# Performance work log

Measured on AMD Instinct MI355X. Metric: run time of the kernel, lower is better.

Reference implementation:

```python
import jax, jax.numpy as jnp
import numpy as np

R, N, E = 6, 50000, 200000
D, H, C, O = 768, 4, 64, 64  # input_dim, heads, hidden_dim1, output_dim


def _gatv2(x, src, tgt, Wl_r, Wr_r, att_r, b_r):
    # PyG GATv2Conv (concat=True, add_self_loops=True, negative_slope=0.2)
    n = x.shape[0]
    xl = (x @ Wl_r).reshape(n, H, C)  # source transform (lin_l)
    xr = (x @ Wr_r).reshape(n, H, C)  # target transform (lin_r)
    loops = jnp.arange(n, dtype=src.dtype)
    s = jnp.concatenate([src, loops])
    t = jnp.concatenate([tgt, loops])
    e = jax.nn.leaky_relu(xl[s] + xr[t], 0.2)          # [E+N, H, C]
    logits = jnp.einsum('ehc,hc->eh', e, att_r)         # [E+N, H]
    m = jax.ops.segment_max(logits, t, num_segments=n)  # softmax over incoming edges
    a = jnp.exp(logits - m[t])
    denom = jax.ops.segment_sum(a, t, num_segments=n)
    alpha = a / (denom[t] + 1e-16)
    msg = xl[s] * alpha[:, :, None]                     # [E+N, H, C]
    out = jax.ops.segment_sum(msg, t, num_segments=n)
    return out.reshape(n, H * C) + b_r


def _graphconv(x, src, tgt, W_rel, W_root, b):
    # PyG GraphConv (aggr='add'): lin_rel(sum_j x_j) + lin_root(x)
    agg = jax.ops.segment_sum(x[src], tgt, num_segments=x.shape[0])
    return agg @ W_rel + b + x @ W_root


def setup_inputs() -> dict:
    key = jax.random.key(0)
    ks = jax.random.split(key, 12)
    s = 0.05
    return {
        'x': jax.random.normal(ks[0], (N, D), jnp.float32),
        'edge_index': jax.random.randint(ks[1], (R, 2, E), 0, N, jnp.int32),
        'Wl': jax.random.normal(ks[2], (R, D, H * C), jnp.float32) * s,
        'Wr': jax.random.normal(ks[3], (R, D, H * C), jnp.float32) * s,
        'att': jax.random.normal(ks[4], (R, H, C), jnp.float32) * s,
        'b_gat': jax.random.normal(ks[5], (R, H * C), jnp.float32) * s,
        'W_rel1': jax.random.normal(ks[6], (R, H * C, C), jnp.float32) * s,
        'W_root1': jax.random.normal(ks[7], (R, H * C, C), jnp.float32) * s,
        'b1': jax.random.normal(ks[8], (R, C), jnp.float32) * s,
        'W_rel2': jax.random.normal(ks[9], (R, C, O), jnp.float32) * s,
        'W_root2': jax.random.normal(ks[10], (R, C, O), jnp.float32) * s,
        'b2': jax.random.normal(ks[11], (R, O), jnp.float32) * s,
    }


def reference(x, edge_index, Wl, Wr, att, b_gat, W_rel1, W_root1, b1, W_rel2, W_root2, b2):
    outs = []
    for r in range(R):  # fixed small set of structurally distinct relation towers
        src, tgt = edge_index[r, 0], edge_index[r, 1]
        h = _gatv2(x, src, tgt, Wl[r], Wr[r], att[r], b_gat[r])
        h = jax.nn.relu(h)
        h = jax.nn.relu(_graphconv(h, src, tgt, W_rel1[r], W_root1[r], b1[r]))
        h = _graphconv(h, src, tgt, W_rel2[r], W_root2[r], b2[r])
        outs.append(h)
    return jnp.stack(outs, axis=1)  # [N, R, O]
```

## Files before the change

kernel.cpp:

```cpp
#include <hip/hip_runtime.h>
#include <hip/hip_bf16.h>
#include <math.h>

#define RREL 6
#define NN   50000
#define EE   200000
#define DD   768
#define HH   4
#define CC   64
#define HC   256
#define OO   64
#define MPAD 50176
#define SCAN_B 49
#define NT   12

typedef __attribute__((ext_vector_type(8))) short short8;
typedef __attribute__((ext_vector_type(4))) float f32x4;
typedef __attribute__((ext_vector_type(8))) unsigned short ushort8v;
typedef __attribute__((ext_vector_type(4))) unsigned short ushort4v;

__device__ __forceinline__ float b2f(unsigned short u) {
  return __uint_as_float(((unsigned)u) << 16);
}
__device__ __forceinline__ unsigned short f2b(float f) {
  __hip_bfloat16 h = __float2bfloat16(f);
  unsigned short u;
  __builtin_memcpy(&u, &h, 2);
  return u;
}

__device__ __forceinline__ void gload16(const void* g, void* s) {
  typedef __attribute__((address_space(1))) void gvoid;
  typedef __attribute__((address_space(3))) void svoid;
  __builtin_amdgcn_global_load_lds((gvoid*)(unsigned long long)g,
                                   (svoid*)(unsigned long long)s, 16, 0, 0);
}

__global__ __launch_bounds__(256) void k_cvt_x(const float* __restrict__ x,
                                               unsigned short* __restrict__ xb) {
  long t = (long)blockIdx.x * 256 + threadIdx.x;
  long base = t * 8;
  int row = (int)(base / DD);
  ushort8v o;
  if (row < NN) {
    float4 a = *(const float4*)(x + base);
    float4 b = *(const float4*)(x + base + 4);
    o[0] = f2b(a.x); o[1] = f2b(a.y); o[2] = f2b(a.z); o[3] = f2b(a.w);
    o[4] = f2b(b.x); o[5] = f2b(b.y); o[6] = f2b(b.z); o[7] = f2b(b.w);
  } else {
    o = (ushort8v)0;
  }
  *(ushort8v*)(xb + base) = o;
}

__global__ __launch_bounds__(256) void k_repack_w(const float* __restrict__ Wl,
                                                  const float* __restrict__ Wr,
                                                  unsigned short* __restrict__ Wt) {
  __shared__ float t[32][33];
  int k0 = blockIdx.x * 32, j0 = blockIdx.y * 32, r = blockIdx.z;
  int tx = threadIdx.x & 31, ty = threadIdx.x >> 5;
#pragma unroll
  for (int s = 0; s < 4; s++) {
    int k = k0 + ty + 8 * s, j = j0 + tx;
    float v = (j < HC) ? Wl[((long)r * DD + k) * HC + j]
                       : Wr[((long)r * DD + k) * HC + (j - HC)];
    t[ty + 8 * s][tx] = v;
  }
  __syncthreads();
#pragma unroll
  for (int s = 0; s < 4; s++) {
    int j = j0 + ty + 8 * s, k = k0 + tx;
    Wt[((long)r * 512 + j) * DD + k] = f2b(t[tx][ty + 8 * s]);
  }
}

__global__ void k_repack_gc(const float* __restrict__ Wrel, const float* __restrict__ Wroot,
                            unsigned short* __restrict__ Bt, int K) {
  int idx = blockIdx.x * blockDim.x + threadIdx.x;
  if (idx >= RREL * 64 * K) return;
  int k = idx % K;
  int o = (idx / K) % 64;
  int r = idx / (64 * K);
  int h = K >> 1;
  float v = (k < h) ? Wrel[((long)r * h + k) * 64 + o]
                    : Wroot[((long)r * h + (k - h)) * 64 + o];
  Bt[idx] = f2b(v);
}

#define STAGE_A(HALF, TT)                                                              \
  if ((TT) < NT) {                                                                     \
    long ko = (long)(TT) * 128;                                                        \
    char* db = ldsA + (((TT) & 1) << 15);                                              \
    gload16(AgB + (long)((HALF) * 64 + rA) * 1536 + ko + xcol,                         \
            db + ((HALF) * 64) * 128 + wave * 1024);                                   \
    gload16(AgB + (long)((HALF) * 64 + 128 + rA) * 1536 + ko + xcol,                   \
            db + ((HALF) * 64 + 128) * 128 + wave * 1024);                             \
  }

#define STAGE_B(HALF, TT)                                                              \
  if ((TT) < NT) {                                                                     \
    long ko = (long)(TT) * 128;                                                        \
    char* db = ldsB + (((TT) & 1) << 15);                                              \
    gload16(BgB + (long)(rb0 + (HALF) * 32 + lane8) * 1536 + ko + xcol,                \
            db + (rb0 + (HALF) * 32) * 128);                                           \
    gload16(BgB + (long)(rb1 + (HALF) * 32 + lane8) * 1536 + ko + xcol,                \
            db + (rb1 + (HALF) * 32) * 128);                                           \
  }

#define RD_PA(MH)                                                                      \
  do {                                                                                 \
    _Pragma("unroll") for (int fi = 0; fi < 4; ++fi) {                                 \
      pa[fi][0] = *(const short8*)(Ard + ((MH) * 64 + fi * 16) * 128 + s0);            \
      pa[fi][1] = *(const short8*)(Ard + ((MH) * 64 + fi * 16) * 128 + s1);            \
    }                                                                                  \
  } while (0)

#define RD_PB(NH)                                                                      \
  do {                                                                                 \
    _Pragma("unroll") for (int fj = 0; fj < 2; ++fj) {                                 \
      pb[fj][0] = *(const short8*)(Brd + ((NH) * 32 + fj * 16) * 128 + s0);            \
      pb[fj][1] = *(const short8*)(Brd + ((NH) * 32 + fj * 16) * 128 + s1);            \
    }                                                                                  \
  } while (0)

#define MM8(MH, NH)                                                                    \
  do {                                                                                 \
    _Pragma("unroll") for (int fi = 0; fi < 4; ++fi)                                   \
    _Pragma("unroll") for (int fj = 0; fj < 2; ++fj) {                                 \
      f32x4 c = acc[(MH) * 4 + fi][(NH) * 2 + fj];                                     \
      c = __builtin_amdgcn_mfma_f32_16x16x32_bf16(pa[fi][0], pb[fj][0], c, 0, 0, 0);   \
      c = __builtin_amdgcn_mfma_f32_16x16x32_bf16(pa[fi][1], pb[fj][1], c, 0, 0, 0);   \
      acc[(MH) * 4 + fi][(NH) * 2 + fj] = c;                                           \
    }                                                                                  \
  } while (0)

__global__ __launch_bounds__(512, 2) void k_gemm(const short* __restrict__ A,
                                                 const short* __restrict__ Bt,
                                                 unsigned short* __restrict__ Yall) {
  __shared__ __align__(16) char ldsA[65536];
  __shared__ __align__(16) char ldsB[65536];
  int tid = threadIdx.x;
  int wgid = blockIdx.x;
  int swz = (wgid & 7) * 294 + (wgid >> 3);
  int bm = swz / 12, bn = swz % 12;
  int lane = tid & 63, wave = tid >> 6;
  int warp_m = wave >> 2, warp_n = wave & 3;
  int wm = warp_m * 128, wn = warp_n * 64;
  int l16 = lane & 15, quad = lane >> 4;
  int gm0 = bm * 256;
  const char* AgB = (const char*)A + (long)gm0 * 1536;
  const char* BgB = (const char*)Bt + (long)bn * 256 * 1536;
  int rA = tid >> 3;
  int lane8 = lane >> 3;
  long xcol = (long)(((tid & 7) ^ (rA & 7)) * 16);
  int rb0 = (wave >> 2) * 64 + (wave & 3) * 8;
  int rb1 = rb0 + 128;
  int s0 = (quad ^ (l16 & 7)) * 16, s1 = s0 ^ 64;
  f32x4 acc[8][4] = {};

  STAGE_A(0, 0); STAGE_B(0, 0); STAGE_A(1, 0); STAGE_B(1, 0);
  STAGE_A(0, 1); STAGE_B(0, 1);
  asm volatile("s_waitcnt vmcnt(4)" ::: "memory");
  __builtin_amdgcn_s_barrier();

  for (int t = 0; t < NT; ++t) {
    int bo = (t & 1) << 15;
    const char* Ard = ldsA + bo + (wm + l16) * 128;
    const char* Brd = ldsB + bo + (wn + l16) * 128;
    short8 pa[4][2], pb[2][2];
    STAGE_A(1, t + 1);
    RD_PA(0); RD_PB(0);
    __builtin_amdgcn_s_barrier();
    asm volatile("s_waitcnt lgkmcnt(0)" ::: "memory");
    __builtin_amdgcn_s_setprio(1); MM8(0, 0); __builtin_amdgcn_s_setprio(0);
    __builtin_amdgcn_s_barrier();
    STAGE_B(1, t + 1);
    RD_PB(1);
    __builtin_amdgcn_s_barrier();
    asm volatile("s_waitcnt lgkmcnt(0)" ::: "memory");
    __builtin_amdgcn_s_setprio(1); MM8(0, 1); __builtin_amdgcn_s_setprio(0);
    __builtin_amdgcn_s_barrier();
    STAGE_A(0, t + 2);
    RD_PA(1); RD_PB(0);
    __builtin_amdgcn_s_barrier();
    asm volatile("s_waitcnt lgkmcnt(0)" ::: "memory");
    __builtin_amdgcn_s_setprio(1); MM8(1, 0); __builtin_amdgcn_s_setprio(0);
    __builtin_amdgcn_s_barrier();
    STAGE_B(0, t + 2);
    RD_PB(1);
    __builtin_amdgcn_s_barrier();
    asm volatile("s_waitcnt lgkmcnt(0)" ::: "memory");
    __builtin_amdgcn_s_setprio(1); MM8(1, 1); __builtin_amdgcn_s_setprio(0);
    if (t < NT - 2)       asm volatile("s_waitcnt vmcnt(4)" ::: "memory");
    else if (t == NT - 2) asm volatile("s_waitcnt vmcnt(0)" ::: "memory");
    __builtin_amdgcn_s_barrier();
  }

  int rel = bn >> 1;
  unsigned short* Yr = Yall + (long)rel * MPAD * 512;
  int cb = (bn & 1) * 256 + wn;
#pragma unroll
  for (int i = 0; i < 8; ++i) {
    int rowb = gm0 + wm + (i >> 2) * 64 + (i & 3) * 16 + quad * 4;
#pragma unroll
    for (int j = 0; j < 4; ++j) {
      int col = cb + (j >> 1) * 32 + (j & 1) * 16 + l16;
#pragma unroll
      for (int reg = 0; reg < 4; ++reg)
        Yr[(long)(rowb + reg) * 512 + col] = f2b(acc[i][j][reg]);
    }
  }
}

template <int K, bool RELU, bool OBF16>
__global__ __launch_bounds__(256) void k_gcgemm(const short* __restrict__ Aall,
                                                const short* __restrict__ Btall,
                                                const float* __restrict__ biasall,
                                                void* __restrict__ outp, long ldo, int ocol,
                                                long orelstride) {
  __shared__ __align__(16) short As[128 * 32];
  __shared__ __align__(16) short Bs[64 * 32];
  int tid = threadIdx.x;
  int bm = blockIdx.x, r = blockIdx.y;
  const short* A  = Aall + (long)r * MPAD * K;
  const short* Bt = Btall + (long)r * 64 * K;
  const float* bias = biasall + (long)r * 64;
  int lane = tid & 63, wave = tid >> 6;
  int quad = lane >> 4, l16 = lane & 15;
  f32x4 acc[2][4] = {};
  const short* Ag = A + (long)bm * 128 * K;
  int lr = lane >> 2, lc = (lane & 3) * 8;
  const short* ga0 = Ag + (long)(wave * 16 + lr) * K + lc;
  const short* ga1 = Ag + (long)(64 + wave * 16 + lr) * K + lc;
  const short* gb0 = Bt + (long)(wave * 16 + lr) * K + lc;
  short* la0 = &As[(wave * 16) * 32];
  short* la1 = &As[(64 + wave * 16) * 32];
  short* lb0 = &Bs[(wave * 16) * 32];
  for (int k0 = 0; k0 < K; k0 += 32) {
    gload16(ga0 + k0, la0);
    gload16(ga1 + k0, la1);
    gload16(gb0 + k0, lb0);
    __syncthreads();
    short8 af[2], bf[4];
#pragma unroll
    for (int i = 0; i < 2; i++) af[i] = *(const short8*)&As[(wave * 32 + i * 16 + l16) * 32 + quad * 8];
#pragma unroll
    for (int j = 0; j < 4; j++) bf[j] = *(const short8*)&Bs[(j * 16 + l16) * 32 + quad * 8];
#pragma unroll
    for (int i = 0; i < 2; i++)
#pragma unroll
      for (int j = 0; j < 4; j++)
        acc[i][j] = __builtin_amdgcn_mfma_f32_16x16x32_bf16(af[i], bf[j], acc[i][j], 0, 0, 0);
    __syncthreads();
  }
#pragma unroll
  for (int i = 0; i < 2; i++)
#pragma unroll
    for (int j = 0; j < 4; j++)
#pragma unroll
      for (int reg = 0; reg < 4; reg++) {
        int row = bm * 128 + wave * 32 + i * 16 + quad * 4 + reg;
        int col = j * 16 + l16;
        float v = acc[i][j][reg] + bias[col];
        if (RELU) v = fmaxf(v, 0.f);
        if (OBF16) {
          ((unsigned short*)outp)[(long)r * orelstride + (long)row * ldo + ocol + col] = f2b(v);
        } else {
          if (row < NN) ((float*)outp)[(long)r * orelstride + (long)row * ldo + ocol + col] = v;
        }
      }
}

__global__ void k_deg6(const int* __restrict__ ei, int* __restrict__ deg6) {
  long e = (long)blockIdx.x * blockDim.x + threadIdx.x;
  if (e >= (long)RREL * EE) return;
  int r = e / EE, i = e % EE;
  int t = ei[(long)r * 2 * EE + EE + i];
  atomicAdd(&deg6[(long)r * NN + t], 1);
}

__global__ __launch_bounds__(256) void k_bsum(const int* __restrict__ deg6, int* __restrict__ bsum) {
  int r = blockIdx.y, b = blockIdx.x, tid = threadIdx.x;
  const int* deg = deg6 + (long)r * NN;
  int i0 = b * 1024 + tid * 4;
  int s = 0;
#pragma unroll
  for (int j = 0; j < 4; j++) { int i = i0 + j; if (i < NN) s += deg[i]; }
#pragma unroll
  for (int m = 1; m < 64; m <<= 1) s += __shfl_xor(s, m);
  __shared__ int ws[4];
  if ((tid & 63) == 0) ws[tid >> 6] = s;
  __syncthreads();
  if (tid == 0) bsum[r * SCAN_B + b] = ws[0] + ws[1] + ws[2] + ws[3];
}

__global__ void k_bscan(int* __restrict__ bsum) {
  int w = threadIdx.x >> 6, l = threadIdx.x & 63;
  int v = (l < SCAN_B) ? bsum[w * SCAN_B + l] : 0;
  int incl = v;
#pragma unroll
  for (int d = 1; d < 64; d <<= 1) { int t = __shfl_up(incl, d); if (l >= d) incl += t; }
  if (l < SCAN_B) bsum[w * SCAN_B + l] = incl - v;
}

__global__ __launch_bounds__(256) void k_boff(const int* __restrict__ deg6, const int* __restrict__ bsum,
                                              int* __restrict__ off6, int* __restrict__ cur6) {
  int r = blockIdx.y, b = blockIdx.x, tid = threadIdx.x;
  const int* deg = deg6 + (long)r * NN;
  int i0 = b * 1024 + tid * 4;
  int v[4], s = 0;
#pragma unroll
  for (int j = 0; j < 4; j++) { int i = i0 + j; v[j] = (i < NN) ? deg[i] : 0; s += v[j]; }
  int l = tid & 63, wv = tid >> 6;
  int incl = s;
#pragma unroll
  for (int d = 1; d < 64; d <<= 1) { int t = __shfl_up(incl, d); if (l >= d) incl += t; }
  __shared__ int ws[4];
  if (l == 63) ws[wv] = incl;
  __syncthreads();
  int pre = incl - s;
  for (int k = 0; k < wv; k++) pre += ws[k];
  pre += bsum[r * SCAN_B + b];
  int e0 = pre;
#pragma unroll
  for (int j = 0; j < 4; j++) {
    int i = i0 + j;
    if (i < NN) { off6[(long)r * NN + i] = e0; cur6[(long)r * NN + i] = e0; }
    e0 += v[j];
  }
}

__global__ void k_scatter6(const int* __restrict__ ei, int* __restrict__ cur6,
                           int* __restrict__ ssrc6) {
  long e = (long)blockIdx.x * blockDim.x + threadIdx.x;
  if (e >= (long)RREL * EE) return;
  int r = e / EE, i = e % EE;
  int src = ei[(long)r * 2 * EE + i];
  int t   = ei[(long)r * 2 * EE + EE + i];
  int p = atomicAdd(&cur6[(long)r * NN + t], 1);
  ssrc6[(long)r * EE + p] = src;
}

__global__ __launch_bounds__(256) void k_gat(unsigned short* __restrict__ Yall,
                                             const int* __restrict__ ssrc6,
                                             const int* __restrict__ off6, const int* __restrict__ deg6,
                                             const float* __restrict__ attall,
                                             const float* __restrict__ bgall) {
  int r = blockIdx.y;
  unsigned short* Y = Yall + (long)r * MPAD * 512;
  const int* ssrc = ssrc6 + (long)r * EE;
  const float* att = attall + r * HC;
  const float* bg  = bgall + r * HC;
  int l = threadIdx.x & 63;
  int n = blockIdx.x * 4 + (threadIdx.x >> 6);
  if (n >= NN) return;
  const unsigned short* yb = Y + (long)n * 512;
  ushort4v xlv = *(const ushort4v*)(yb + 4 * l);
  ushort4v xrv = *(const ushort4v*)(yb + 256 + 4 * l);
  float xl[4], xr[4];
#pragma unroll
  for (int j = 0; j < 4; j++) { xl[j] = b2f(xlv[j]); xr[j] = b2f(xrv[j]); }
  float4 at4 = *(const float4*)(att + 4 * l);
  float at[4] = {at4.x, at4.y, at4.z, at4.w};
  float num[4] = {0.f, 0.f, 0.f, 0.f}, den = 0.f;
  {
    float lg = 0.f;
#pragma unroll
    for (int j = 0; j < 4; j++) {
      float e = xl[j] + xr[j];
      e = e > 0.f ? e : 0.2f * e;
      lg += at[j] * e;
    }
    lg += __shfl_xor(lg, 1); lg += __shfl_xor(lg, 2);
    lg += __shfl_xor(lg, 4); lg += __shfl_xor(lg, 8);
    float a = expf(lg);
    den += a;
#pragma unroll
    for (int j = 0; j < 4; j++) num[j] += a * xl[j];
  }
  int st = off6[(long)r * NN + n], cnt = deg6[(long)r * NN + n];
  int i = 0;
  for (; i + 2 <= cnt; i += 2) {
    int s0 = ssrc[st + i], s1 = ssrc[st + i + 1];
    ushort4v v0 = *(const ushort4v*)(Y + (long)s0 * 512 + 4 * l);
    ushort4v v1 = *(const ushort4v*)(Y + (long)s1 * 512 + 4 * l);
    float x0[4], x1[4];
#pragma unroll
    for (int j = 0; j < 4; j++) { x0[j] = b2f(v0[j]); x1[j] = b2f(v1[j]); }
    float lg0 = 0.f, lg1 = 0.f;
#pragma unroll
    for (int j = 0; j < 4; j++) {
      float e0 = x0[j] + xr[j]; e0 = e0 > 0.f ? e0 : 0.2f * e0; lg0 += at[j] * e0;
      float e1 = x1[j] + xr[j]; e1 = e1 > 0.f ? e1 : 0.2f * e1; lg1 += at[j] * e1;
    }
    lg0 += __shfl_xor(lg0, 1); lg1 += __shfl_xor(lg1, 1);
    lg0 += __shfl_xor(lg0, 2); lg1 += __shfl_xor(lg1, 2);
    lg0 += __shfl_xor(lg0, 4); lg1 += __shfl_xor(lg1, 4);
    lg0 += __shfl_xor(lg0, 8); lg1 += __shfl_xor(lg1, 8);
    float a0 = expf(lg0), a1 = expf(lg1);
    den += a0 + a1;
#pragma unroll
    for (int j = 0; j < 4; j++) num[j] += a0 * x0[j] + a1 * x1[j];
  }
  if (i < cnt) {
    int s0 = ssrc[st + i];
    ushort4v v0 = *(const ushort4v*)(Y + (long)s0 * 512 + 4 * l);
    float x0[4];
#pragma unroll
    for (int j = 0; j < 4; j++) x0[j] = b2f(v0[j]);
    float lg = 0.f;
#pragma unroll
    for (int j = 0; j < 4; j++) {
      float e = x0[j] + xr[j];
      e = e > 0.f ? e : 0.2f * e;
      lg += at[j] * e;
    }
    lg += __shfl_xor(lg, 1); lg += __shfl_xor(lg, 2);
    lg += __shfl_xor(lg, 4); lg += __shfl_xor(lg, 8);
    float a = expf(lg);
    den += a;
#pragma unroll
    for (int j = 0; j < 4; j++) num[j] += a * x0[j];
  }
  float4 bg4 = *(const float4*)(bg + 4 * l);
  float bgj[4] = {bg4.x, bg4.y, bg4.z, bg4.w};
  ushort4v o;
  float inv = 1.f / (den + 1e-16f);
#pragma unroll
  for (int j = 0; j < 4; j++) o[j] = f2b(fmaxf(num[j] * inv + bgj[j], 0.f));
  *(ushort4v*)(Y + (long)n * 512 + 256 + 4 * l) = o;
}

__global__ __launch_bounds__(256) void k_agg1(unsigned short* __restrict__ Yall,
                                              const int* __restrict__ ssrc6,
                                              const int* __restrict__ off6,
                                              const int* __restrict__ deg6) {
  int r = blockIdx.y;
  unsigned short* Y = Yall + (long)r * MPAD * 512;
  const int* ssrc = ssrc6 + (long)r * EE;
  int l = threadIdx.x & 63;
  int n = blockIdx.x * 4 + (threadIdx.x >> 6);
  if (n >= NN) return;
  float acc[4] = {0.f, 0.f, 0.f, 0.f};
  int st = off6[(long)r * NN + n], cnt = deg6[(long)r * NN + n];
  int i = 0;
  for (; i + 4 <= cnt; i += 4) {
    int s0 = ssrc[st + i], s1 = ssrc[st + i + 1], s2 = ssrc[st + i + 2], s3 = ssrc[st + i + 3];
    ushort4v v0 = *(const ushort4v*)(Y + (long)s0 * 512 + 256 + 4 * l);
    ushort4v v1 = *(const ushort4v*)(Y + (long)s1 * 512 + 256 + 4 * l);
    ushort4v v2 = *(const ushort4v*)(Y + (long)s2 * 512 + 256 + 4 * l);
    ushort4v v3 = *(const ushort4v*)(Y + (long)s3 * 512 + 256 + 4 * l);
#pragma unroll
    for (int j = 0; j < 4; j++)
      acc[j] += b2f(v0[j]) + b2f(v1[j]) + b2f(v2[j]) + b2f(v3[j]);
  }
  for (; i < cnt; i++) {
    int s = ssrc[st + i];
    ushort4v v = *(const ushort4v*)(Y + (long)s * 512 + 256 + 4 * l);
#pragma unroll
    for (int j = 0; j < 4; j++) acc[j] += b2f(v[j]);
  }
  ushort4v o;
#pragma unroll
  for (int j = 0; j < 4; j++) o[j] = f2b(acc[j]);
  *(ushort4v*)(Y + (long)n * 512 + 4 * l) = o;
}

__global__ __launch_bounds__(256) void k_agg2(unsigned short* __restrict__ ABall,
                                              const int* __restrict__ ssrc6,
                                              const int* __restrict__ off6,
                                              const int* __restrict__ deg6) {
  int r = blockIdx.y;
  unsigned short* AB2 = ABall + (long)r * MPAD * 128;
  const int* ssrc = ssrc6 + (long)r * EE;
  int l = threadIdx.x & 63;
  int n = blockIdx.x * 4 + (threadIdx.x >> 6);
  if (n >= NN) return;
  float acc = 0.f;
  int st = off6[(long)r * NN + n], cnt = deg6[(long)r * NN + n];
  int i = 0;
  for (; i + 4 <= cnt; i += 4) {
    int s0 = ssrc[st + i], s1 = ssrc[st + i + 1], s2 = ssrc[st + i + 2], s3 = ssrc[st + i + 3];
    acc += b2f(AB2[(long)s0 * 128 + OO + l]) + b2f(AB2[(long)s1 * 128 + OO + l]) +
           b2f(AB2[(long)s2 * 128 + OO + l]) + b2f(AB2[(long)s3 * 128 + OO + l]);
  }
  for (; i < cnt; i++) {
    int s = ssrc[st + i];
    acc += b2f(AB2[(long)s * 128 + OO + l]);
  }
  AB2[(long)n * 128 + l] = f2b(acc);
}

extern "C" void kernel_launch(void* const* d_in, const int* in_sizes, int n_in,
                              void* d_out, int out_size, void* d_ws, size_t ws_size,
                              hipStream_t stream) {
  (void)in_sizes; (void)n_in; (void)out_size;
  const float* x      = (const float*)d_in[0];
  const int*   ei     = (const int*)d_in[1];
  const float* Wl     = (const float*)d_in[2];
  const float* Wr     = (const float*)d_in[3];
  const float* att    = (const float*)d_in[4];
  const float* bg     = (const float*)d_in[5];
  const float* Wrel1  = (const float*)d_in[6];
  const float* Wroot1 = (const float*)d_in[7];
  const float* b1     = (const float*)d_in[8];
  const float* Wrel2  = (const float*)d_in[9];
  const float* Wroot2 = (const float*)d_in[10];
  const float* b2     = (const float*)d_in[11];
  float* out = (float*)d_out;

  char* ws = (char*)d_ws;
  size_t ofs = 0;
  auto alloc = [&](size_t bytes) {
    char* p = ws + ofs;
    ofs += (bytes + 255) & ~(size_t)255;
    return p;
  };
  unsigned short* Xb   = (unsigned short*)alloc((size_t)MPAD * DD * 2);
  unsigned short* Wt   = (unsigned short*)alloc((size_t)RREL * 512 * DD * 2);
  unsigned short* Wt1  = (unsigned short*)alloc((size_t)RREL * 64 * 512 * 2);
  unsigned short* Wt2  = (unsigned short*)alloc((size_t)RREL * 64 * 128 * 2);
  unsigned short* Yall = (unsigned short*)alloc((size_t)RREL * MPAD * 512 * 2);
  unsigned short* AB2  = (unsigned short*)alloc((size_t)RREL * MPAD * 128 * 2);
  int* deg6   = (int*)alloc((size_t)RREL * NN * 4);
  int* off6   = (int*)alloc((size_t)RREL * NN * 4);
  int* cur6   = (int*)alloc((size_t)RREL * NN * 4);
  int* bsum   = (int*)alloc((size_t)RREL * SCAN_B * 4);
  int* ssrc6  = (int*)alloc((size_t)RREL * EE * 4);
  if (ofs > ws_size) return;

  k_cvt_x<<<(int)((long)MPAD * DD / 8 / 256), 256, 0, stream>>>(x, Xb);
  k_repack_w<<<dim3(DD / 32, 512 / 32, RREL), 256, 0, stream>>>(Wl, Wr, Wt);
  k_repack_gc<<<(RREL * 64 * 512 + 255) / 256, 256, 0, stream>>>(Wrel1, Wroot1, Wt1, 512);
  k_repack_gc<<<(RREL * 64 * 128 + 255) / 256, 256, 0, stream>>>(Wrel2, Wroot2, Wt2, 128);
  hipMemsetAsync(deg6, 0, (size_t)RREL * NN * 4, stream);
  k_deg6<<<((long)RREL * EE + 255) / 256, 256, 0, stream>>>(ei, deg6);
  k_bsum<<<dim3(SCAN_B, RREL), 256, 0, stream>>>(deg6, bsum);
  k_bscan<<<1, 384, 0, stream>>>(bsum);
  k_boff<<<dim3(SCAN_B, RREL), 256, 0, stream>>>(deg6, bsum, off6, cur6);
  k_scatter6<<<((long)RREL * EE + 255) / 256, 256, 0, stream>>>(ei, cur6, ssrc6);

  k_gemm<<<dim3(196 * 12), 512, 0, stream>>>((const short*)Xb, (const short*)Wt, Yall);
  k_gat<<<dim3(NN / 4, RREL), 256, 0, stream>>>(Yall, ssrc6, off6, deg6, att, bg);
  k_agg1<<<dim3(NN / 4, RREL), 256, 0, stream>>>(Yall, ssrc6, off6, deg6);
  k_gcgemm<512, true, true><<<dim3(MPAD / 128, RREL), 256, 0, stream>>>(
      (const short*)Yall, (const short*)Wt1, b1, (void*)AB2, 128, OO, (long)MPAD * 128);
  k_agg2<<<dim3(NN / 4, RREL), 256, 0, stream>>>(AB2, ssrc6, off6, deg6);
  k_gcgemm<128, false, false><<<dim3(MPAD / 128, RREL), 256, 0, stream>>>(
      (const short*)AB2, (const short*)Wt2, b2, (void*)out, RREL * OO, 0, 64);
}
```

Baseline: 1.229 ms.

## Restructure GEMM K-loop to load B fragments once and cut barriers

Reworks the k_gemm main loop. Both halves of each wave's B fragments are now read from LDS once per K tile and reused for both M halves. The second A-half fragment reads are issued between MFMA groups so they overlap with math. The global staging for the next tiles is grouped into two points, which removes several block-wide barriers and lgkmcnt waits per iteration. The cost is more live fragment registers (pa0, pa1, pb), which may pressure occupancy at 512 threads with 2 blocks per CU.

```diff
diff --git a/kernel.cpp b/kernel.cpp
--- a/kernel.cpp
+++ b/kernel.cpp
@@ -107,30 +107,14 @@
             db + (rb1 + (HALF) * 32) * 128);                                           \
   }
 
-#define RD_PA(MH)                                                                      \
-  do {                                                                                 \
-    _Pragma("unroll") for (int fi = 0; fi < 4; ++fi) {                                 \
-      pa[fi][0] = *(const short8*)(Ard + ((MH) * 64 + fi * 16) * 128 + s0);            \
-      pa[fi][1] = *(const short8*)(Ard + ((MH) * 64 + fi * 16) * 128 + s1);            \
-    }                                                                                  \
-  } while (0)
-
-#define RD_PB(NH)                                                                      \
-  do {                                                                                 \
-    _Pragma("unroll") for (int fj = 0; fj < 2; ++fj) {                                 \
-      pb[fj][0] = *(const short8*)(Brd + ((NH) * 32 + fj * 16) * 128 + s0);            \
-      pb[fj][1] = *(const short8*)(Brd + ((NH) * 32 + fj * 16) * 128 + s1);            \
-    }                                                                                  \
-  } while (0)
-
-#define MM8(MH, NH)                                                                    \
+#define MMQ(PA, AOFF, NH)                                                              \
   do {                                                                                 \
     _Pragma("unroll") for (int fi = 0; fi < 4; ++fi)                                   \
     _Pragma("unroll") for (int fj = 0; fj < 2; ++fj) {                                 \
-      f32x4 c = acc[(MH) * 4 + fi][(NH) * 2 + fj];                                     \
-      c = __builtin_amdgcn_mfma_f32_16x16x32_bf16(pa[fi][0], pb[fj][0], c, 0, 0, 0);   \
-      c = __builtin_amdgcn_mfma_f32_16x16x32_bf16(pa[fi][1], pb[fj][1], c, 0, 0, 0);   \
-      acc[(MH) * 4 + fi][(NH) * 2 + fj] = c;                                           \
+      f32x4 c = acc[(AOFF) + fi][(NH) * 2 + fj];                                       \
+      c = __builtin_amdgcn_mfma_f32_16x16x32_bf16(PA[fi][0], pb[NH][fj][0], c, 0, 0, 0);\
+      c = __builtin_amdgcn_mfma_f32_16x16x32_bf16(PA[fi][1], pb[NH][fj][1], c, 0, 0, 0);\
+      acc[(AOFF) + fi][(NH) * 2 + fj] = c;                                             \
     }                                                                                  \
   } while (0)
 
@@ -167,30 +151,42 @@
     int bo = (t & 1) << 15;
     const char* Ard = ldsA + bo + (wm + l16) * 128;
     const char* Brd = ldsB + bo + (wn + l16) * 128;
-    short8 pa[4][2], pb[2][2];
+    short8 pa0[4][2], pa1[4][2], pb[2][2][2];
     STAGE_A(1, t + 1);
-    RD_PA(0); RD_PB(0);
+    STAGE_B(1, t + 1);
+#pragma unroll
+    for (int fi = 0; fi < 4; ++fi) {
+      pa0[fi][0] = *(const short8*)(Ard + (fi * 16) * 128 + s0);
+      pa0[fi][1] = *(const short8*)(Ard + (fi * 16) * 128 + s1);
+    }
+#pragma unroll
+    for (int nh = 0; nh < 2; ++nh)
+#pragma unroll
+      for (int fj = 0; fj < 2; ++fj) {
+        pb[nh][fj][0] = *(const short8*)(Brd + (nh * 32 + fj * 16) * 128 + s0);
+        pb[nh][fj][1] = *(const short8*)(Brd + (nh * 32 + fj * 16) * 128 + s1);
+      }
     __builtin_amdgcn_s_barrier();
     asm volatile("s_waitcnt lgkmcnt(0)" ::: "memory");
-    __builtin_amdgcn_s_setprio(1); MM8(0, 0); __builtin_amdgcn_s_setprio(0);
-    __builtin_amdgcn_s_barrier();
-    STAGE_B(1, t + 1);
-    RD_PB(1);
-    __builtin_amdgcn_s_barrier();
-    asm volatile("s_waitcnt lgkmcnt(0)" ::: "memory");
-    __builtin_amdgcn_s_setprio(1); MM8(0, 1); __builtin_amdgcn_s_setprio(0);
+    __builtin_amdgcn_s_setprio(1);
+    MMQ(pa0, 0, 0);
+    __builtin_amdgcn_s_setprio(0);
+#pragma unroll
+    for (int fi = 0; fi < 4; ++fi) {
+      pa1[fi][0] = *(const short8*)(Ard + ((64 + fi * 16)) * 128 + s0);
+      pa1[fi][1] = *(const short8*)(Ard + ((64 + fi * 16)) * 128 + s1);
+    }
+    __builtin_amdgcn_s_setprio(1);
+    MMQ(pa0, 0, 1);
+    __builtin_amdgcn_s_setprio(0);
     __builtin_amdgcn_s_barrier();
     STAGE_A(0, t + 2);
-    RD_PA(1); RD_PB(0);
-    __builtin_amdgcn_s_barrier();
+    STAGE_B(0, t + 2);
     asm volatile("s_waitcnt lgkmcnt(0)" ::: "memory");
-    __builtin_amdgcn_s_setprio(1); MM8(1, 0); __builtin_amdgcn_s_setprio(0);
-    __builtin_amdgcn_s_barrier();
-    STAGE_B(0, t + 2);
-    RD_PB(1);
-    __builtin_amdgcn_s_barrier();
-    asm volatile("s_waitcnt lgkmcnt(0)" ::: "memory");
-    __builtin_amdgcn_s_setprio(1); MM8(1, 1); __builtin_amdgcn_s_setprio(0);
+    __builtin_amdgcn_s_setprio(1);
+    MMQ(pa1, 4, 0);
+    MMQ(pa1, 4, 1);
+    __builtin_amdgcn_s_setprio(0);
     if (t < NT - 2)       asm volatile("s_waitcnt vmcnt(4)" ::: "memory");
     else if (t == NT - 2) asm volatile("s_waitcnt vmcnt(0)" ::: "memory");
     __builtin_amdgcn_s_barrier();
```

Measured after the change: 1.210 ms. No clear change (-1.5%).
